# Optimization experiments

Measured on AMD Instinct MI355X. Metric: run time of the kernel, lower is better.

Reference implementation:

```python
import jax, jax.numpy as jnp
import numpy as np

B, IN, MEM, CTX, H = 8192, 1024, 1024, 1024, 4
DH = CTX // H

def setup_inputs() -> dict:
    key = jax.random.key(0)
    ks = jax.random.split(key, 20)
    s = 0.02
    d = {
        'input_tensor': jax.random.normal(ks[0], (B, IN), jnp.float32),
        'previous_memory': jax.random.normal(ks[1], (B, MEM), jnp.float32),
        # MultiheadAttention packed in_proj (q,k,v) and out_proj
        'in_proj_w': jax.random.normal(ks[2], (3 * CTX, CTX), jnp.float32) * s,
        'in_proj_b': jnp.zeros((3 * CTX,), jnp.float32),
        'out_proj_w': jax.random.normal(ks[3], (CTX, CTX), jnp.float32) * s,
        'out_proj_b': jnp.zeros((CTX,), jnp.float32),
        # input/memory projections
        'ip_w': jax.random.normal(ks[4], (CTX, IN), jnp.float32) * s,
        'ip_b': jnp.zeros((CTX,), jnp.float32),
        'mp_w': jax.random.normal(ks[5], (CTX, MEM), jnp.float32) * s,
        'mp_b': jnp.zeros((CTX,), jnp.float32),
        # forget / output gates
        'fg_w': jax.random.normal(ks[6], (MEM, MEM + IN), jnp.float32) * s,
        'fg_b': jnp.zeros((MEM,), jnp.float32),
        'og_w': jax.random.normal(ks[7], (MEM, MEM), jnp.float32) * s,
        'og_b': jnp.zeros((MEM,), jnp.float32),
        # GRUCell weights (PyTorch layout: [3*hidden, in], gates order r,z,n)
        'gru_w_ih': jax.random.normal(ks[8], (3 * MEM, CTX), jnp.float32) * s,
        'gru_b_ih': jnp.zeros((3 * MEM,), jnp.float32),
        'gru_w_hh': jax.random.normal(ks[9], (3 * MEM, MEM), jnp.float32) * s,
        'gru_b_hh': jnp.zeros((3 * MEM,), jnp.float32),
    }
    return d

def _forward(input_tensor, previous_memory, in_proj_w, in_proj_b, out_proj_w, out_proj_b,
             ip_w, ip_b, mp_w, mp_b, fg_w, fg_b, og_w, og_b,
             gru_w_ih, gru_b_ih, gru_w_hh, gru_b_hh):
    # projections
    pi = input_tensor @ ip_w.T + ip_b          # [B, CTX] (query; also context/value)
    pm = previous_memory @ mp_w.T + mp_b       # [B, CTX] (key)
    # MHA with q_len = kv_len = 1: softmax over a single key -> weights = 1
    wq, wk, wv = jnp.split(in_proj_w, 3, axis=0)
    bq, bk, bv = jnp.split(in_proj_b, 3, axis=0)
    q = (pi @ wq.T + bq).reshape(B, H, DH)
    k = (pm @ wk.T + bk).reshape(B, H, DH)
    v = (pi @ wv.T + bv).reshape(B, H, DH)
    scores = jnp.sum(q * k, axis=-1, keepdims=True) / jnp.sqrt(jnp.float32(DH))  # [B,H,1]
    w = jax.nn.softmax(scores, axis=-1)        # all ones (single key)
    attn = (w * v).reshape(B, CTX)             # == v
    context_aware = attn @ out_proj_w.T + out_proj_b  # [B, CTX]
    attention_weights = jnp.mean(w, axis=1)[:, None, :]  # [B,1,1], avg over heads
    # forget gate
    forget_in = jnp.concatenate([previous_memory, input_tensor], axis=-1)
    fgate = jax.nn.sigmoid(forget_in @ fg_w.T + fg_b)
    gated_mem = previous_memory * fgate
    # GRUCell (PyTorch semantics)
    gi = context_aware @ gru_w_ih.T + gru_b_ih
    gh = gated_mem @ gru_w_hh.T + gru_b_hh
    gi_r, gi_z, gi_n = jnp.split(gi, 3, axis=-1)
    gh_r, gh_z, gh_n = jnp.split(gh, 3, axis=-1)
    r = jax.nn.sigmoid(gi_r + gh_r)
    z = jax.nn.sigmoid(gi_z + gh_z)
    n = jnp.tanh(gi_n + r * gh_n)
    updated = (1.0 - z) * n + z * gated_mem
    ogate = jax.nn.sigmoid(updated @ og_w.T + og_b)
    return updated * ogate, attention_weights

def reference(input_tensor, previous_memory, in_proj_w, in_proj_b, out_proj_w, out_proj_b,
              ip_w, ip_b, mp_w, mp_b, fg_w, fg_b, og_w, og_b,
              gru_w_ih, gru_b_ih, gru_w_hh, gru_b_hh):
    return _forward(input_tensor, previous_memory, in_proj_w, in_proj_b, out_proj_w, out_proj_b,
                    ip_w, ip_b, mp_w, mp_b, fg_w, fg_b, og_w, og_b,
                    gru_w_ih, gru_b_ih, gru_w_hh, gru_b_hh)
```

## Files before the change

### kernel.cpp

```cpp
#include <hip/hip_runtime.h>
#include <cstdint>
#include <cstddef>


typedef __bf16 bf16;
typedef bf16 bf16x4 __attribute__((ext_vector_type(4)));
typedef bf16 bf16x8 __attribute__((ext_vector_type(8)));
typedef float f32x4 __attribute__((ext_vector_type(4)));

#define B_ROWS 8192

__device__ __forceinline__ float sigmoid_f(float x) {
    return 1.0f / (1.0f + __expf(-x));
}
__device__ __forceinline__ float tanh_f(float x) {
    return 1.0f - 2.0f / (__expf(2.0f * x) + 1.0f);
}

template <int EPI>
__device__ __forceinline__ void g256_core(
    bf16* lds,
    const bf16* A1, int lda1, const bf16* W1, int ldw1, int nt1,
    const bf16* A2, int lda2, const bf16* W2, int ldw2, int nt2,
    const float* bias1, const float* bias2,
    int N, int brow, int bcol,
    bf16* out_bf, float* out_f32,
    const float* aux_f32, const bf16* aux_bf,
    const bf16* grz, const bf16* gni, const bf16* gat)
{
    bf16* sA = lds;
    bf16* sB = lds + 3 * 256 * 32;

    const int tid  = threadIdx.x;
    const int lane = tid & 63;
    const int wave = tid >> 6;
    const int wm   = wave >> 1;
    const int wn   = wave & 1;
    const int lrow = lane & 15;
    const int lq   = lane >> 4;

    f32x4 acc[8][4];
#pragma unroll
    for (int i = 0; i < 8; ++i)
#pragma unroll
        for (int j = 0; j < 4; ++j) {
            f32x4 z = {0.0f, 0.0f, 0.0f, 0.0f};
            acc[i][j] = z;
        }

    auto stage = [&](bf16* dA, bf16* dB, int kt) {
        const bf16* Ab; int lda; const bf16* Wb; int ldw; int k0;
        if (kt < nt1) { Ab = A1; lda = lda1; Wb = W1; ldw = ldw1; k0 = kt << 5; }
        else          { Ab = A2; lda = lda2; Wb = W2; ldw = ldw2; k0 = (kt - nt1) << 5; }
#pragma unroll
        for (int i = 0; i < 4; ++i) {
            const int s   = tid + i * 256;
            const int row = s >> 2;
            const int col = (((s & 3) ^ ((s >> 3) & 3)) << 3);
            const bf16* gp = Ab + (size_t)(brow + row) * lda + (k0 + col);
            __builtin_amdgcn_global_load_lds(
                (const __attribute__((address_space(1))) void*)gp,
                (__attribute__((address_space(3))) void*)(&dA[s * 8]),
                16, 0, 0);
        }
#pragma unroll
        for (int i = 0; i < 2; ++i) {
            const int s   = tid + i * 256;
            const int row = s >> 2;
            const int col = (((s & 3) ^ ((s >> 3) & 3)) << 3);
            const bf16* gp = Wb + (size_t)(bcol + row) * ldw + (k0 + col);
            __builtin_amdgcn_global_load_lds(
                (const __attribute__((address_space(1))) void*)gp,
                (__attribute__((address_space(3))) void*)(&dB[s * 8]),
                16, 0, 0);
        }
    };

    const int NT = nt1 + nt2;

    bf16* a0 = sA;           bf16* b0 = sB;
    bf16* a1 = sA + 8192;    bf16* b1 = sB + 4096;
    bf16* a2 = sA + 16384;   bf16* b2 = sB + 8192;

    stage(a0, b0, 0);
    stage(a1, b1, 1);
    asm volatile("s_waitcnt vmcnt(6)" ::: "memory");
    __builtin_amdgcn_s_barrier();
    __builtin_amdgcn_sched_barrier(0);

    for (int kt = 0; kt < NT; ++kt) {
        bf16x8 av[8], bv[4];
#pragma unroll
        for (int i = 0; i < 8; ++i) {
            const int r = wm * 128 + i * 16 + lrow;
            av[i] = *(const bf16x8*)&a0[r * 32 + ((lq ^ ((r >> 1) & 3)) << 3)];
        }
#pragma unroll
        for (int j = 0; j < 4; ++j) {
            const int r = wn * 64 + j * 16 + lrow;
            bv[j] = *(const bf16x8*)&b0[r * 32 + ((lq ^ ((r >> 1) & 3)) << 3)];
        }

        stage(a2, b2, kt + 2 < NT ? kt + 2 : NT - 1);

#pragma unroll
        for (int i = 0; i < 8; ++i)
#pragma unroll
            for (int j = 0; j < 4; ++j)
                acc[i][j] = __builtin_amdgcn_mfma_f32_16x16x32_bf16(
                    av[i], bv[j], acc[i][j], 0, 0, 0);

        __builtin_amdgcn_sched_barrier(0);
        asm volatile("s_waitcnt vmcnt(6)" ::: "memory");
        __builtin_amdgcn_s_barrier();
        __builtin_amdgcn_sched_barrier(0);

        bf16* ta = a0; a0 = a1; a1 = a2; a2 = ta;
        bf16* tb = b0; b0 = b1; b1 = b2; b2 = tb;
    }

    asm volatile("s_waitcnt vmcnt(0)" ::: "memory");
    __syncthreads();

    if constexpr (EPI == 0) {
        bf16* cb = lds;
#pragma unroll
        for (int j = 0; j < 4; ++j) {
            const int col = wn * 64 + j * 16 + lrow;
            float bj = bias1[bcol + col];
            if (bias2) bj += bias2[bcol + col];
#pragma unroll
            for (int i = 0; i < 8; ++i) {
                const int rowb = wm * 128 + i * 16 + lq * 4;
#pragma unroll
                for (int r = 0; r < 4; ++r)
                    cb[(rowb + r) * 136 + col] = (bf16)(acc[i][j][r] + bj);
            }
        }
        __syncthreads();
#pragma unroll
        for (int p = 0; p < 16; ++p) {
            const int row = p * 16 + (tid >> 4);
            const int col = (tid & 15) * 8;
            bf16x8 v = *(const bf16x8*)&cb[row * 136 + col];
            *(bf16x8*)&out_bf[(size_t)(brow + row) * N + bcol + col] = v;
        }
    } else {
        float* cf = (float*)lds;
#pragma unroll
        for (int h = 0; h < 2; ++h) {
            if (wm == h) {
#pragma unroll
                for (int j = 0; j < 4; ++j) {
                    const int col = wn * 64 + j * 16 + lrow;
                    const float bj = bias1[bcol + col];
#pragma unroll
                    for (int i = 0; i < 8; ++i) {
                        const int rl = i * 16 + lq * 4;
#pragma unroll
                        for (int r = 0; r < 4; ++r)
                            cf[(rl + r) * 132 + col] = acc[i][j][r] + bj;
                    }
                }
            }
            __syncthreads();
#pragma unroll
            for (int p = 0; p < 16; ++p) {
                const int idx = p * 256 + tid;
                const int row = idx >> 5;
                const int ch  = idx & 31;
                f32x4 v = *(const f32x4*)&cf[row * 132 + ch * 4];
                const int grow = brow + h * 128 + row;
                const int gcol = bcol + ch * 4;
                const size_t gidx = (size_t)grow * N + gcol;
                if constexpr (EPI == 1) {
                    f32x4 a4 = *(const f32x4*)&aux_f32[gidx];
                    bf16x4 o;
#pragma unroll
                    for (int e = 0; e < 4; ++e)
                        o[e] = (bf16)(a4[e] * sigmoid_f(v[e]));
                    *(bf16x4*)&out_bf[gidx] = o;
                } else if constexpr (EPI == 2) {
                    bf16x4 ab = *(const bf16x4*)&aux_bf[gidx];
                    f32x4 o;
#pragma unroll
                    for (int e = 0; e < 4; ++e)
                        o[e] = (float)ab[e] * sigmoid_f(v[e]);
                    *(f32x4*)&out_f32[gidx] = o;
                } else {
                    const bf16* pr = grz + (size_t)grow * 2048 + gcol;
                    bf16x4 rr = *(const bf16x4*)pr;
                    bf16x4 zz = *(const bf16x4*)(pr + 1024);
                    bf16x4 g4 = *(const bf16x4*)&gni[gidx];
                    bf16x4 m4 = *(const bf16x4*)&gat[gidx];
                    bf16x4 o;
#pragma unroll
                    for (int e = 0; e < 4; ++e) {
                        const float r = sigmoid_f((float)rr[e]);
                        const float z = sigmoid_f((float)zz[e]);
                        const float n = tanh_f((float)g4[e] + r * v[e]);
                        o[e] = (bf16)((1.0f - z) * n + z * (float)m4[e]);
                    }
                    *(bf16x4*)&out_bf[gidx] = o;
                }
            }
            __syncthreads();
        }
    }
}

template <int BM>
__device__ __forceinline__ void gemm_core_tb(
    bf16* sA, bf16* sB,
    const bf16* __restrict__ A, int lda,
    const bf16* __restrict__ W, int ldw,
    const float* __restrict__ bias,
    int N, int K, int brow, int bcol, int epi,
    bf16* __restrict__ out_bf, int tld)
{
    constexpr int AI = BM / 32;
    const int tid  = threadIdx.x;
    const int lane = tid & 63;
    const int wave = tid >> 6;
    const int wr   = (wave & 1) * (BM / 2);
    const int wc   = (wave >> 1) * 64;
    const int lrow = lane & 15;
    const int lq   = lane >> 4;

    f32x4 acc[AI][4];
#pragma unroll
    for (int i = 0; i < AI; ++i)
#pragma unroll
        for (int j = 0; j < 4; ++j) {
            f32x4 z = {0.0f, 0.0f, 0.0f, 0.0f};
            acc[i][j] = z;
        }

    auto stage = [&](bf16* dA, bf16* dB, int k0) {
#pragma unroll
        for (int i = 0; i < BM / 64; ++i) {
            const int s   = tid + i * 256;
            const int row = s >> 2;
            const int col = (((s & 3) ^ ((s >> 3) & 3)) << 3);
            const bf16* gp = A + (size_t)(brow + row) * lda + (k0 + col);
            __builtin_amdgcn_global_load_lds(
                (const __attribute__((address_space(1))) void*)gp,
                (__attribute__((address_space(3))) void*)(&dA[s * 8]),
                16, 0, 0);
        }
#pragma unroll
        for (int i = 0; i < 2; ++i) {
            const int s   = tid + i * 256;
            const int row = s >> 2;
            const int col = (((s & 3) ^ ((s >> 3) & 3)) << 3);
            const bf16* gp = W + (size_t)(bcol + row) * ldw + (k0 + col);
            __builtin_amdgcn_global_load_lds(
                (const __attribute__((address_space(1))) void*)gp,
                (__attribute__((address_space(3))) void*)(&dB[s * 8]),
                16, 0, 0);
        }
    };

#define WAIT_LPS()                                                   \
    do {                                                             \
        if constexpr (BM == 128)                                     \
            asm volatile("s_waitcnt vmcnt(4)" ::: "memory");         \
        else                                                         \
            asm volatile("s_waitcnt vmcnt(3)" ::: "memory");         \
    } while (0)

    const int NT = K >> 5;

    bf16* a0 = sA;               bf16* b0 = sB;
    bf16* a1 = sA + BM * 32;     bf16* b1 = sB + 4096;
    bf16* a2 = sA + 2 * BM * 32; bf16* b2 = sB + 2 * 4096;

    stage(a0, b0, 0);
    stage(a1, b1, NT > 1 ? 32 : 0);
    WAIT_LPS();
    __builtin_amdgcn_s_barrier();
    __builtin_amdgcn_sched_barrier(0);

    for (int kt = 0; kt < NT; ++kt) {
        bf16x8 av[AI], bv[4];
#pragma unroll
        for (int i = 0; i < AI; ++i) {
            const int r = wr + i * 16 + lrow;
            av[i] = *(const bf16x8*)&a0[r * 32 + ((lq ^ ((r >> 1) & 3)) << 3)];
        }
#pragma unroll
        for (int j = 0; j < 4; ++j) {
            const int r = wc + j * 16 + lrow;
            bv[j] = *(const bf16x8*)&b0[r * 32 + ((lq ^ ((r >> 1) & 3)) << 3)];
        }

        const int kn = (kt + 2 < NT ? kt + 2 : NT - 1) << 5;
        stage(a2, b2, kn);

#pragma unroll
        for (int i = 0; i < AI; ++i)
#pragma unroll
            for (int j = 0; j < 4; ++j)
                acc[i][j] = __builtin_amdgcn_mfma_f32_16x16x32_bf16(
                    av[i], bv[j], acc[i][j], 0, 0, 0);

        __builtin_amdgcn_sched_barrier(0);
        WAIT_LPS();
        __builtin_amdgcn_s_barrier();
        __builtin_amdgcn_sched_barrier(0);

        bf16* ta = a0; a0 = a1; a1 = a2; a2 = ta;
        bf16* tb = b0; b0 = b1; b1 = b2; b2 = tb;
    }

    asm volatile("s_waitcnt vmcnt(0)" ::: "memory");
#undef WAIT_LPS

#pragma unroll
    for (int j = 0; j < 4; ++j) {
        const int gcol = bcol + wc + j * 16 + lrow;
        const float bj = bias ? bias[gcol] : 0.0f;
#pragma unroll
        for (int i = 0; i < AI; ++i) {
            const int growb = brow + wr + i * 16 + lq * 4;
#pragma unroll
            for (int r = 0; r < 4; ++r) {
                const int grow = growb + r;
                const float val = acc[i][j][r] + bj;
                if (epi == 0) {
                    out_bf[(size_t)grow * N + gcol] = (bf16)val;
                } else {
                    out_bf[(size_t)gcol * tld + grow] = (bf16)val;
                }
            }
        }
    }
}

__device__ __forceinline__ void gemv_rows(
    const float* __restrict__ W, const float* __restrict__ x,
    const float* __restrict__ b, float* __restrict__ y, int nbase)
{
    const int n    = nbase + (threadIdx.x >> 6);
    const int lane = threadIdx.x & 63;
    const float* row = W + (size_t)n * 1024;
    float s = 0.0f;
    for (int k = lane * 4; k < 1024; k += 256) {
        f32x4 w = *(const f32x4*)(row + k);
        f32x4 xv = *(const f32x4*)(x + k);
        s += w[0] * xv[0] + w[1] * xv[1] + w[2] * xv[2] + w[3] * xv[3];
    }
#pragma unroll
    for (int off = 32; off; off >>= 1) s += __shfl_down(s, off);
    if (lane == 0) y[n] = s + b[n];
}

__global__ void prep_k(
    const float* __restrict__ prev, const float* __restrict__ input,
    bf16* __restrict__ cat,
    const float* __restrict__ wv, const float* __restrict__ wop,
    const float* __restrict__ wih, const float* __restrict__ wfg,
    const float* __restrict__ wog, const float* __restrict__ whh,
    bf16* __restrict__ dv, bf16* __restrict__ dop, bf16* __restrict__ dih,
    bf16* __restrict__ dfg, bf16* __restrict__ dog, bf16* __restrict__ dhh,
    const float* __restrict__ ipw, bf16* __restrict__ wipt,
    float* __restrict__ ones,
    const float* __restrict__ ip_b, const float* __restrict__ bv,
    float* __restrict__ t1b)
{
    __shared__ float t[32][33];
    const int b = blockIdx.x;
    if (b < 16384) {
        const int i = b * 256 + threadIdx.x;
        const int row = i >> 9;
        const int c4  = i & 511;
        f32x4 v;
        if (c4 < 256)
            v = ((const f32x4*)prev)[(size_t)row * 256 + c4];
        else
            v = ((const f32x4*)input)[(size_t)row * 256 + (c4 - 256)];
        bf16x4 o = {(bf16)v[0], (bf16)v[1], (bf16)v[2], (bf16)v[3]};
        ((bf16x4*)cat)[i] = o;
    } else if (b < 27648) {
        const int c = (b - 16384) * 256 + threadIdx.x;
        const float* s; bf16* d; int o;
        if (c < 262144)        { s = wv;  d = dv;  o = c; }
        else if (c < 524288)   { s = wop; d = dop; o = c - 262144; }
        else if (c < 1310720)  { s = wih; d = dih; o = c - 524288; }
        else if (c < 1835008)  { s = wfg; d = dfg; o = c - 1310720; }
        else if (c < 2097152)  { s = wog; d = dog; o = c - 1835008; }
        else                   { s = whh; d = dhh; o = c - 2097152; }
        f32x4 v = ((const f32x4*)s)[o];
        bf16x4 w = {(bf16)v[0], (bf16)v[1], (bf16)v[2], (bf16)v[3]};
        ((bf16x4*)d)[o] = w;
    } else if (b < 28672) {
        const int b2 = b - 27648;
        const int bx = (b2 & 31) * 32;
        const int by = (b2 >> 5) * 32;
        const int tx = threadIdx.x & 31, ty = threadIdx.x >> 5;
#pragma unroll
        for (int i = 0; i < 32; i += 8)
            t[ty + i][tx] = ipw[(size_t)(by + ty + i) * 1024 + bx + tx];
        __syncthreads();
#pragma unroll
        for (int i = 0; i < 32; i += 8)
            wipt[(size_t)(bx + ty + i) * 1024 + by + tx] = (bf16)t[tx][ty + i];
    } else if (b < 28680) {
        const int i = (b - 28672) * 256 + threadIdx.x;
        if (i < 2048) {
            f32x4 one = {1.0f, 1.0f, 1.0f, 1.0f};
            ((f32x4*)ones)[i] = one;
        }
    } else {
        gemv_rows(wv, ip_b, bv, t1b, (b - 28680) * 4);
    }
}

__global__ __launch_bounds__(256, 2) void comb1_k(
    const bf16* __restrict__ wvb, const bf16* __restrict__ wipt,
    bf16* __restrict__ t1t,
    const float* __restrict__ wop_f, const float* __restrict__ t1b,
    const float* __restrict__ bop, float* __restrict__ t2b,
    const bf16* __restrict__ cat, const bf16* __restrict__ wfgb,
    const float* __restrict__ fg_b, const float* __restrict__ prev,
    bf16* __restrict__ gated)
{
    __shared__ bf16 lds[36864];
    const int b = blockIdx.x;
    if (b < 128) {
        const int by = b % 16, bx = b / 16;
        gemm_core_tb<64>(lds, lds + 3 * 64 * 32, wvb, 1024, wipt, 1024,
                         nullptr, 1024, 1024, by * 64, bx * 128, 3, t1t, 1024);
    } else if (b < 384) {
        gemv_rows(wop_f, t1b, bop, t2b, (b - 128) * 4);
    } else {
        const int id = b - 384;
        const int by = id & 31, bx = id >> 5;
        g256_core<1>(lds, cat, 2048, wfgb, 2048, 64,
                     nullptr, 0, nullptr, 0, 0,
                     fg_b, nullptr, 1024, by * 256, bx * 128,
                     gated, nullptr, prev, nullptr, nullptr, nullptr, nullptr);
    }
}

__global__ __launch_bounds__(256, 2) void comb2_k(
    const bf16* __restrict__ wopb, const bf16* __restrict__ t1t,
    bf16* __restrict__ t2t,
    const float* __restrict__ wih_f, const float* __restrict__ t2b,
    const float* __restrict__ bih, float* __restrict__ t3b)
{
    __shared__ bf16 lds[36864];
    const int b = blockIdx.x;
    if (b < 128) {
        const int by = b % 16, bx = b / 16;
        gemm_core_tb<64>(lds, lds + 3 * 64 * 32, wopb, 1024, t1t, 1024,
                         nullptr, 1024, 1024, by * 64, bx * 128, 3, t2t, 1024);
    } else {
        gemv_rows(wih_f, t2b, bih, t3b, (b - 128) * 4);
    }
}

__global__ __launch_bounds__(256, 2) void gemm64_k(
    const bf16* __restrict__ A, const bf16* __restrict__ W,
    bf16* __restrict__ out_bf)
{
    __shared__ bf16 sA[3 * 64 * 32];
    __shared__ bf16 sB[3 * 128 * 32];
    const int by = blockIdx.x % 48;
    const int bx = blockIdx.x / 48;
    gemm_core_tb<64>(sA, sB, A, 1024, W, 1024, nullptr,
                     1024, 1024, by * 64, bx * 128, 0, out_bf, 0);
}

__global__ __launch_bounds__(256, 2) void big_k(
    const bf16* __restrict__ x, const bf16* __restrict__ wcomb,
    const bf16* __restrict__ gated, const bf16* __restrict__ whh,
    const float* __restrict__ t3b, const float* __restrict__ bhh,
    bf16* __restrict__ grz,
    const bf16* __restrict__ wcomb_n, const float* __restrict__ bias_n,
    bf16* __restrict__ gni)
{
    __shared__ bf16 lds[36864];
    const int b = blockIdx.x;
    if (b < 512) {
        const int by = b & 31, bx = b >> 5;
        g256_core<0>(lds, x, 2048, wcomb, 1024, 32,
                     gated, 1024, whh, 1024, 32,
                     t3b, bhh, 2048, by * 256, bx * 128,
                     grz, nullptr, nullptr, nullptr, nullptr, nullptr, nullptr);
    } else {
        const int id = b - 512;
        const int by = id & 31, bx = id >> 5;
        g256_core<0>(lds, x, 2048, wcomb_n, 1024, 32,
                     nullptr, 0, nullptr, 0, 0,
                     bias_n, nullptr, 1024, by * 256, bx * 128,
                     gni, nullptr, nullptr, nullptr, nullptr, nullptr, nullptr);
    }
}

__global__ __launch_bounds__(256, 2) void g3_k(
    const bf16* __restrict__ gated, const bf16* __restrict__ whh_n,
    const float* __restrict__ bhh_n,
    const bf16* __restrict__ grz, const bf16* __restrict__ gni,
    bf16* __restrict__ upd)
{
    __shared__ bf16 lds[36864];
    const int by = blockIdx.x & 31, bx = blockIdx.x >> 5;
    g256_core<4>(lds, gated, 1024, whh_n, 1024, 32,
                 nullptr, 0, nullptr, 0, 0,
                 bhh_n, nullptr, 1024, by * 256, bx * 128,
                 upd, nullptr, nullptr, nullptr, grz, gni, gated);
}

__global__ __launch_bounds__(256, 2) void og_k(
    const bf16* __restrict__ upd, const bf16* __restrict__ wog,
    const float* __restrict__ og_b, float* __restrict__ out)
{
    __shared__ bf16 lds[36864];
    const int by = blockIdx.x & 31, bx = blockIdx.x >> 5;
    g256_core<2>(lds, upd, 1024, wog, 1024, 32,
                 nullptr, 0, nullptr, 0, 0,
                 og_b, nullptr, 1024, by * 256, bx * 128,
                 nullptr, out, nullptr, upd, nullptr, nullptr, nullptr);
}

extern "C" void kernel_launch(void* const* d_in, const int* in_sizes, int n_in,
                              void* d_out, int out_size, void* d_ws,
                              size_t ws_size, hipStream_t stream) {
    const float* input      = (const float*)d_in[0];
    const float* prev       = (const float*)d_in[1];
    const float* in_proj_w  = (const float*)d_in[2];
    const float* in_proj_b  = (const float*)d_in[3];
    const float* out_proj_w = (const float*)d_in[4];
    const float* out_proj_b = (const float*)d_in[5];
    const float* ip_w       = (const float*)d_in[6];
    const float* ip_b       = (const float*)d_in[7];
    const float* fg_w  = (const float*)d_in[10];
    const float* fg_b  = (const float*)d_in[11];
    const float* og_w  = (const float*)d_in[12];
    const float* og_b  = (const float*)d_in[13];
    const float* gih_w = (const float*)d_in[14];
    const float* gih_b = (const float*)d_in[15];
    const float* ghh_w = (const float*)d_in[16];
    const float* ghh_b = (const float*)d_in[17];
    float* out = (float*)d_out;

    char* ws = (char*)d_ws;
    const size_t MB = 1024 * 1024;
    bf16* CAT   = (bf16*)(ws);
    bf16* WHHB  = (bf16*)(ws + 32 * MB);
    bf16* GRZ   = (bf16*)(ws + 38 * MB);
    bf16* GNI   = (bf16*)(ws + 70 * MB);
    bf16* GATED = (bf16*)(ws + 86 * MB);
    bf16* UPD   = (bf16*)(ws + 102 * MB);
    bf16* WCOMB = (bf16*)(ws + 118 * MB);
    bf16* WOGB  = (bf16*)(ws + 124 * MB);
    bf16* WFGB  = (bf16*)(ws + 126 * MB);
    bf16* WVB   = (bf16*)(ws + 130 * MB);
    bf16* WOPB  = (bf16*)(ws + 132 * MB);
    bf16* WIHB  = (bf16*)(ws + 134 * MB);
    bf16* WIPT  = (bf16*)(ws + 140 * MB);
    bf16* T1T   = (bf16*)(ws + 142 * MB);
    bf16* T2T   = (bf16*)(ws + 144 * MB);
    float* T1B  = (float*)(ws + 146 * MB);
    float* T2B  = (float*)(ws + 146 * MB + 8192);
    float* T3B  = (float*)(ws + 146 * MB + 16384);

    const int M = B_ROWS;
    dim3 blk(256);

    prep_k<<<dim3(28936), blk, 0, stream>>>(
        prev, input, CAT,
        in_proj_w + 2048 * 1024, out_proj_w, gih_w, fg_w, og_w, ghh_w,
        WVB, WOPB, WIHB, WFGB, WOGB, WHHB,
        ip_w, WIPT, out + (size_t)M * 1024,
        ip_b, in_proj_b + 2048, T1B);
    comb1_k<<<dim3(640), blk, 0, stream>>>(
        WVB, WIPT, T1T,
        out_proj_w, T1B, out_proj_b, T2B,
        CAT, WFGB, fg_b, prev, GATED);
    comb2_k<<<dim3(896), blk, 0, stream>>>(
        WOPB, T1T, T2T,
        gih_w, T2B, gih_b, T3B);
    gemm64_k<<<dim3(384), blk, 0, stream>>>(WIHB, T2T, WCOMB);
    big_k<<<dim3(768), blk, 0, stream>>>(
        CAT + 1024, WCOMB, GATED, WHHB, T3B, ghh_b, GRZ,
        WCOMB + (size_t)2048 * 1024, T3B + 2048, GNI);
    g3_k<<<dim3(256), blk, 0, stream>>>(
        GATED, WHHB + (size_t)2048 * 1024, ghh_b + 2048, GRZ, GNI, UPD);
    og_k<<<dim3(256), blk, 0, stream>>>(UPD, WOGB, og_b, out);
}
```

Baseline: 434.6 us.

## Reassociate weight-product chain to remove a dependent GEMM launch

The combined weight W_ih·W_op·W_v·W_ip was computed as three sequential dependent GEMMs. It is now computed as (W_ih·W_op) in parallel with (W_v·W_ip), followed by a single product of the two, so one kernel launch and one serial stage disappear. W_op is now transposed to bf16 in the prep kernel instead of being converted directly. The workspace layout is shuffled to fit the new intermediate P. The extra cost is that the first stage does the larger 3072x1024 GEMM alongside the others, which makes that kernel heavier.

```diff
diff --git a/kernel.cpp b/kernel.cpp
--- a/kernel.cpp
+++ b/kernel.cpp
@@ -361,9 +361,10 @@
     const float* __restrict__ wv, const float* __restrict__ wop,
     const float* __restrict__ wih, const float* __restrict__ wfg,
     const float* __restrict__ wog, const float* __restrict__ whh,
-    bf16* __restrict__ dv, bf16* __restrict__ dop, bf16* __restrict__ dih,
+    bf16* __restrict__ dv, bf16* __restrict__ dih,
     bf16* __restrict__ dfg, bf16* __restrict__ dog, bf16* __restrict__ dhh,
     const float* __restrict__ ipw, bf16* __restrict__ wipt,
+    bf16* __restrict__ wopt,
     float* __restrict__ ones,
     const float* __restrict__ ip_b, const float* __restrict__ bv,
     float* __restrict__ t1b)
@@ -381,30 +382,32 @@
             v = ((const f32x4*)input)[(size_t)row * 256 + (c4 - 256)];
         bf16x4 o = {(bf16)v[0], (bf16)v[1], (bf16)v[2], (bf16)v[3]};
         ((bf16x4*)cat)[i] = o;
-    } else if (b < 27648) {
+    } else if (b < 26624) {
         const int c = (b - 16384) * 256 + threadIdx.x;
         const float* s; bf16* d; int o;
         if (c < 262144)        { s = wv;  d = dv;  o = c; }
-        else if (c < 524288)   { s = wop; d = dop; o = c - 262144; }
-        else if (c < 1310720)  { s = wih; d = dih; o = c - 524288; }
-        else if (c < 1835008)  { s = wfg; d = dfg; o = c - 1310720; }
-        else if (c < 2097152)  { s = wog; d = dog; o = c - 1835008; }
-        else                   { s = whh; d = dhh; o = c - 2097152; }
+        else if (c < 1048576)  { s = wih; d = dih; o = c - 262144; }
+        else if (c < 1572864)  { s = wfg; d = dfg; o = c - 1048576; }
+        else if (c < 1835008)  { s = wog; d = dog; o = c - 1572864; }
+        else                   { s = whh; d = dhh; o = c - 1835008; }
         f32x4 v = ((const f32x4*)s)[o];
         bf16x4 w = {(bf16)v[0], (bf16)v[1], (bf16)v[2], (bf16)v[3]};
         ((bf16x4*)d)[o] = w;
     } else if (b < 28672) {
-        const int b2 = b - 27648;
-        const int bx = (b2 & 31) * 32;
-        const int by = (b2 >> 5) * 32;
+        const int b2 = b - 26624;
+        const float* src = (b2 < 1024) ? ipw : wop;
+        bf16* dst = (b2 < 1024) ? wipt : wopt;
+        const int b3 = b2 & 1023;
+        const int bx = (b3 & 31) * 32;
+        const int by = (b3 >> 5) * 32;
         const int tx = threadIdx.x & 31, ty = threadIdx.x >> 5;
 #pragma unroll
         for (int i = 0; i < 32; i += 8)
-            t[ty + i][tx] = ipw[(size_t)(by + ty + i) * 1024 + bx + tx];
+            t[ty + i][tx] = src[(size_t)(by + ty + i) * 1024 + bx + tx];
         __syncthreads();
 #pragma unroll
         for (int i = 0; i < 32; i += 8)
-            wipt[(size_t)(bx + ty + i) * 1024 + by + tx] = (bf16)t[tx][ty + i];
+            dst[(size_t)(bx + ty + i) * 1024 + by + tx] = (bf16)t[tx][ty + i];
     } else if (b < 28680) {
         const int i = (b - 28672) * 256 + threadIdx.x;
         if (i < 2048) {
@@ -419,6 +422,8 @@
 __global__ __launch_bounds__(256, 2) void comb1_k(
     const bf16* __restrict__ wvb, const bf16* __restrict__ wipt,
     bf16* __restrict__ t1t,
+    const bf16* __restrict__ wihb, const bf16* __restrict__ wopt,
+    bf16* __restrict__ p,
     const float* __restrict__ wop_f, const float* __restrict__ t1b,
     const float* __restrict__ bop, float* __restrict__ t2b,
     const bf16* __restrict__ cat, const bf16* __restrict__ wfgb,
@@ -431,10 +436,15 @@
         const int by = b % 16, bx = b / 16;
         gemm_core_tb<64>(lds, lds + 3 * 64 * 32, wvb, 1024, wipt, 1024,
                          nullptr, 1024, 1024, by * 64, bx * 128, 3, t1t, 1024);
-    } else if (b < 384) {
-        gemv_rows(wop_f, t1b, bop, t2b, (b - 128) * 4);
+    } else if (b < 512) {
+        const int id = b - 128;
+        const int by = id % 48, bx = id / 48;
+        gemm_core_tb<64>(lds, lds + 3 * 64 * 32, wihb, 1024, wopt, 1024,
+                         nullptr, 1024, 1024, by * 64, bx * 128, 0, p, 0);
+    } else if (b < 768) {
+        gemv_rows(wop_f, t1b, bop, t2b, (b - 512) * 4);
     } else {
-        const int id = b - 384;
+        const int id = b - 768;
         const int by = id & 31, bx = id >> 5;
         g256_core<1>(lds, cat, 2048, wfgb, 2048, 64,
                      nullptr, 0, nullptr, 0, 0,
@@ -444,32 +454,20 @@
 }
 
 __global__ __launch_bounds__(256, 2) void comb2_k(
-    const bf16* __restrict__ wopb, const bf16* __restrict__ t1t,
-    bf16* __restrict__ t2t,
+    const bf16* __restrict__ p, const bf16* __restrict__ t1t,
+    bf16* __restrict__ wcomb,
     const float* __restrict__ wih_f, const float* __restrict__ t2b,
     const float* __restrict__ bih, float* __restrict__ t3b)
 {
     __shared__ bf16 lds[36864];
     const int b = blockIdx.x;
-    if (b < 128) {
-        const int by = b % 16, bx = b / 16;
-        gemm_core_tb<64>(lds, lds + 3 * 64 * 32, wopb, 1024, t1t, 1024,
-                         nullptr, 1024, 1024, by * 64, bx * 128, 3, t2t, 1024);
+    if (b < 384) {
+        const int by = b % 48, bx = b / 48;
+        gemm_core_tb<64>(lds, lds + 3 * 64 * 32, p, 1024, t1t, 1024,
+                         nullptr, 1024, 1024, by * 64, bx * 128, 0, wcomb, 0);
     } else {
-        gemv_rows(wih_f, t2b, bih, t3b, (b - 128) * 4);
-    }
-}
-
-__global__ __launch_bounds__(256, 2) void gemm64_k(
-    const bf16* __restrict__ A, const bf16* __restrict__ W,
-    bf16* __restrict__ out_bf)
-{
-    __shared__ bf16 sA[3 * 64 * 32];
-    __shared__ bf16 sB[3 * 128 * 32];
-    const int by = blockIdx.x % 48;
-    const int bx = blockIdx.x / 48;
-    gemm_core_tb<64>(sA, sB, A, 1024, W, 1024, nullptr,
-                     1024, 1024, by * 64, bx * 128, 0, out_bf, 0);
+        gemv_rows(wih_f, t2b, bih, t3b, (b - 384) * 4);
+    }
 }
 
 __global__ __launch_bounds__(256, 2) void big_k(
@@ -557,14 +555,14 @@
     bf16* WOGB  = (bf16*)(ws + 124 * MB);
     bf16* WFGB  = (bf16*)(ws + 126 * MB);
     bf16* WVB   = (bf16*)(ws + 130 * MB);
-    bf16* WOPB  = (bf16*)(ws + 132 * MB);
+    float* T1B  = (float*)(ws + 132 * MB);
+    float* T2B  = (float*)(ws + 132 * MB + 8192);
+    float* T3B  = (float*)(ws + 132 * MB + 16384);
     bf16* WIHB  = (bf16*)(ws + 134 * MB);
     bf16* WIPT  = (bf16*)(ws + 140 * MB);
     bf16* T1T   = (bf16*)(ws + 142 * MB);
-    bf16* T2T   = (bf16*)(ws + 144 * MB);
-    float* T1B  = (float*)(ws + 146 * MB);
-    float* T2B  = (float*)(ws + 146 * MB + 8192);
-    float* T3B  = (float*)(ws + 146 * MB + 16384);
+    bf16* WOPT  = (bf16*)(ws + 144 * MB);
+    bf16* P     = (bf16*)(ws + 146 * MB);
 
     const int M = B_ROWS;
     dim3 blk(256);
@@ -572,17 +570,17 @@
     prep_k<<<dim3(28936), blk, 0, stream>>>(
         prev, input, CAT,
         in_proj_w + 2048 * 1024, out_proj_w, gih_w, fg_w, og_w, ghh_w,
-        WVB, WOPB, WIHB, WFGB, WOGB, WHHB,
-        ip_w, WIPT, out + (size_t)M * 1024,
+        WVB, WIHB, WFGB, WOGB, WHHB,
+        ip_w, WIPT, WOPT, out + (size_t)M * 1024,
         ip_b, in_proj_b + 2048, T1B);
-    comb1_k<<<dim3(640), blk, 0, stream>>>(
+    comb1_k<<<dim3(1024), blk, 0, stream>>>(
         WVB, WIPT, T1T,
+        WIHB, WOPT, P,
         out_proj_w, T1B, out_proj_b, T2B,
         CAT, WFGB, fg_b, prev, GATED);
-    comb2_k<<<dim3(896), blk, 0, stream>>>(
-        WOPB, T1T, T2T,
+    comb2_k<<<dim3(1152), blk, 0, stream>>>(
+        P, T1T, WCOMB,
         gih_w, T2B, gih_b, T3B);
-    gemm64_k<<<dim3(384), blk, 0, stream>>>(WIHB, T2T, WCOMB);
     big_k<<<dim3(768), blk, 0, stream>>>(
         CAT + 1024, WCOMB, GATED, WHHB, T3B, ghh_b, GRZ,
         WCOMB + (size_t)2048 * 1024, T3B + 2048, GNI);
```

Measured after the change: 586.4 us. +34.9%, slower.
